# Kernel optimization log

Measured on AMD Instinct MI355X. Metric: run time of the kernel, lower is better.

## Reference

```python
import jax, jax.numpy as jnp
import numpy as np

D_HEAD = 64
KV_GROUPS = 3
KSIZE = 7


def _win_idx(L, ksize):
    # NATTEN neighborhood: window centered at i, shifted to stay in-bounds.
    start = jnp.clip(jnp.arange(L) - ksize // 2, 0, L - ksize)  # [L]
    return start[:, None] + jnp.arange(ksize)[None, :]          # [L, k]


def _natten2d(q, k, v, ksize):
    # q,k,v: [n, nh, H, W, e]; q pre-scaled.
    H, W = q.shape[2], q.shape[3]
    ih = _win_idx(H, ksize)  # [H, k]
    iw = _win_idx(W, ksize)  # [W, k]
    # gather per-query key/value windows: [n, nh, H, W, k, k, e]
    kg = k[:, :, ih[:, None, :, None], iw[None, :, None, :], :]
    vg = v[:, :, ih[:, None, :, None], iw[None, :, None, :], :]
    logits = jnp.einsum('nhije,nhijabe->nhijab', q, kg)  # [n,nh,H,W,k,k]
    n_, nh = logits.shape[:2]
    a = jax.nn.softmax(logits.reshape(n_, nh, H, W, ksize * ksize), axis=-1)
    a = a.reshape(logits.shape)
    return jnp.einsum('nhijab,nhijabe->nhije', a, vg)  # [n,nh,H,W,e]


def _to_heads(p, nh, e):
    n, h, w, _ = p.shape
    return p.reshape(n, h, w, nh, e).transpose(0, 3, 1, 2, 4)  # [n,nh,h,w,e]


def setup_inputs() -> dict:
    key = jax.random.key(0)
    k1, k2, k3 = jax.random.split(key, 3)
    x = jax.random.normal(k1, (2, 32, 32, 768), dtype=jnp.float32)
    w_qkv = jax.random.normal(k2, (1280, 768), dtype=jnp.float32) * 0.02
    w_out = jax.random.normal(k3, (768, 768), dtype=jnp.float32) * 0.02
    return {"x": x, "w_qkv": w_qkv, "w_out": w_out}


def reference(x, w_qkv, w_out):
    n, H, W, d_model = x.shape
    q_heads = d_model // D_HEAD
    kv_heads = q_heads // KV_GROUPS
    qkv = x @ w_qkv.T  # [n,H,W,1280]
    q, k, v = jnp.split(
        qkv, [q_heads * D_HEAD, (q_heads + kv_heads) * D_HEAD], axis=-1)
    q = _to_heads(q, q_heads, D_HEAD)
    k = jnp.tile(_to_heads(k, kv_heads, D_HEAD), (1, KV_GROUPS, 1, 1, 1))
    v = jnp.tile(_to_heads(v, kv_heads, D_HEAD), (1, KV_GROUPS, 1, 1, 1))
    q = q / (D_HEAD ** 0.5)
    o = _natten2d(q, k, v, KSIZE)           # [n,nh,H,W,e]
    o = o.transpose(0, 2, 3, 1, 4).reshape(n, H, W, d_model)
    return o @ w_out.T
```

## Files before the change

kernel.cpp:

```cpp
#include <hip/hip_runtime.h>
#include <hip/hip_bf16.h>


typedef __attribute__((ext_vector_type(8))) __bf16 bf16x8;
typedef __attribute__((ext_vector_type(4))) float floatx4;
typedef unsigned short u16;

__device__ inline u16 f2bf(float f) {
    union { float f; unsigned u; } v; v.f = f;
    return (u16)((v.u + 0x7fff + ((v.u >> 16) & 1)) >> 16);
}

__device__ inline void gl_lds16(const void* g, void* l) {
    __builtin_amdgcn_global_load_lds(
        (const __attribute__((address_space(1))) void*)g,
        (__attribute__((address_space(3))) void*)l, 16, 0, 0);
}

__global__ __launch_bounds__(256) void convert_kernel(
    const float* __restrict__ x, const float* __restrict__ w1,
    const float* __restrict__ w2, u16* __restrict__ xb,
    u16* __restrict__ w1b, u16* __restrict__ w2b)
{
    int t = blockIdx.x * blockDim.x + threadIdx.x;
    const float* s; u16* d;
    if (t < 393216)      { s = x;  d = xb; }
    else if (t < 638976) { s = w1; d = w1b; t -= 393216; }
    else                 { s = w2; d = w2b; t -= 638976; }
    float4 v = ((const float4*)s)[t];
    ushort4 o;
    o.x = f2bf(v.x); o.y = f2bf(v.y); o.z = f2bf(v.z); o.w = f2bf(v.w);
    ((ushort4*)d)[t] = o;
}

template<int MODE>
__global__ __launch_bounds__(256) void gemm_nt(
    const u16* __restrict__ A, const u16* __restrict__ B,
    float* __restrict__ C, u16* __restrict__ Cb, u16* __restrict__ vT,
    int M, int N, int K)
{
    __shared__ __align__(16) u16 As[4 * 64 * 32];
    __shared__ __align__(16) u16 Bs[4 * 64 * 32];
    const int tid = threadIdx.x;
    const int lane = tid & 63;
    const int wave = tid >> 6;
    const int bm = blockIdx.y * 64;
    const int bn = blockIdx.x * 64;
    const int qr = (wave >> 1) * 32;
    const int qc = (wave & 1) * 32;

    floatx4 acc[2][2] = {};

    const u16* Xsrc = (wave < 2) ? A : B;
    const int   bx  = (wave < 2) ? bm : bn;
    u16* Xlds       = (wave < 2) ? As : Bs;
    const int half  = wave & 1;
    const int l2 = lane >> 2;
    const int l3 = (lane & 3) * 8;
    const u16* gptr[8];
    u16* lptr[8];
    #pragma unroll
    for (int cc = 0; cc < 8; cc++) {
        int c = half * 8 + cc, kc = c & 3, rg = c >> 2;
        gptr[cc] = Xsrc + (size_t)(bx + rg * 16 + l2) * K + kc * 32 + l3;
        lptr[cc] = Xlds + kc * 2048 + rg * 512;
    }

    const int fr = lane & 15;
    const int fk = (lane >> 4) * 8;

    for (int k0 = 0; k0 < K; k0 += 128) {
        #pragma unroll
        for (int cc = 0; cc < 8; cc++)
            gl_lds16(gptr[cc] + k0, lptr[cc]);
        __syncthreads();
        #pragma unroll
        for (int kc = 0; kc < 4; kc++) {
            bf16x8 af0 = *(const bf16x8*)&As[kc * 2048 + (qr +      fr) * 32 + fk];
            bf16x8 af1 = *(const bf16x8*)&As[kc * 2048 + (qr + 16 + fr) * 32 + fk];
            bf16x8 bf0 = *(const bf16x8*)&Bs[kc * 2048 + (qc +      fr) * 32 + fk];
            bf16x8 bf1 = *(const bf16x8*)&Bs[kc * 2048 + (qc + 16 + fr) * 32 + fk];
            acc[0][0] = __builtin_amdgcn_mfma_f32_16x16x32_bf16(af0, bf0, acc[0][0], 0, 0, 0);
            acc[0][1] = __builtin_amdgcn_mfma_f32_16x16x32_bf16(af0, bf1, acc[0][1], 0, 0, 0);
            acc[1][0] = __builtin_amdgcn_mfma_f32_16x16x32_bf16(af1, bf0, acc[1][0], 0, 0, 0);
            acc[1][1] = __builtin_amdgcn_mfma_f32_16x16x32_bf16(af1, bf1, acc[1][1], 0, 0, 0);
        }
        __syncthreads();
    }

    const int cr = (lane >> 4) * 4;
    const int ccol = lane & 15;
    #pragma unroll
    for (int i = 0; i < 2; i++) {
        #pragma unroll
        for (int j = 0; j < 2; j++) {
            const int row0 = bm + qr + i * 16 + cr;
            const int col  = bn + qc + j * 16 + ccol;
            if (MODE == 0) {
                #pragma unroll
                for (int r = 0; r < 4; r++)
                    C[(size_t)(row0 + r) * N + col] = acc[i][j][r];
            } else {
                if (col < 1024) {
                    #pragma unroll
                    for (int r = 0; r < 4; r++)
                        Cb[(size_t)(row0 + r) * 1024 + col] = f2bf(acc[i][j][r]);
                } else {
                    ushort4 w;
                    w.x = f2bf(acc[i][j][0]); w.y = f2bf(acc[i][j][1]);
                    w.z = f2bf(acc[i][j][2]); w.w = f2bf(acc[i][j][3]);
                    *(ushort4*)&vT[(size_t)(col - 1024) * 2048 + row0] = w;
                }
            }
        }
    }
}

__global__ __launch_bounds__(256) void natten_mfma(
    const u16* __restrict__ qkv, const u16* __restrict__ vT,
    u16* __restrict__ o)
{
    __shared__ __align__(16) u16 Ks[224 * 72];
    __shared__ __align__(16) u16 Vs[64 * 224];
    __shared__ __align__(16) u16 Pw[4 * 512];
    const int h  = blockIdx.x;
    const int tb = blockIdx.y;
    const int g  = h & 3;
    const int batch = tb >> 4;
    const int ti = ((tb >> 2) & 3) * 8;
    const int tj = (tb & 3) * 8;
    const int wu_i = min(max(ti - 3, 0), 18);
    const int wu_j = min(max(tj - 3, 0), 18);
    const int tid = threadIdx.x, lane = tid & 63, wave = tid >> 6;
    const int pixbase = batch << 10;

    for (int c = tid; c < 1792; c += 256) {
        int n = c >> 3, seg = (c & 7) * 8;
        int a = n >> 4, b = min(n & 15, 13);
        int pix = pixbase + (wu_i + a) * 32 + wu_j + b;
        *(uint4*)&Ks[n * 72 + seg] =
            *(const uint4*)&qkv[(size_t)pix * 1024 + 768 + g * 64 + seg];
    }
    {
        const int b  = lane & 15;
        const int ar = lane >> 4;
        bool vok[4]; int voff[4];
        #pragma unroll
        for (int rr = 0; rr < 4; rr++) {
            int a = ar + rr * 4;
            vok[rr]  = (a < 14) && (b < 14);
            voff[rr] = (wu_i + a) * 32 + wu_j + b;
        }
        const u16* vsrc = &vT[(size_t)(g * 64 + wave * 16) * 2048 + pixbase];
        #pragma unroll 4
        for (int dd = 0; dd < 16; dd++) {
            #pragma unroll
            for (int rr = 0; rr < 4; rr++) {
                int a = ar + rr * 4;
                if (a < 14)
                    Vs[(wave * 16 + dd) * 224 + rr * 64 + lane] =
                        vok[rr] ? vsrc[voff[rr]] : (u16)0;
            }
            vsrc += 2048;
        }
    }
    __syncthreads();

    const int fr = lane & 15;
    const int fk = (lane >> 4) * 8;

    bf16x8 aq0, aq1;
    {
        int qq = wave * 16 + fr;
        int pixq = pixbase + (ti + (qq >> 3)) * 32 + tj + (qq & 7);
        const u16* qp = &qkv[(size_t)pixq * 1024 + h * 64];
        aq0 = *(const bf16x8*)(qp + fk);
        aq1 = *(const bf16x8*)(qp + 32 + fk);
    }

    bool colok[4]; int tlo[4], thi[4];
    #pragma unroll
    for (int r = 0; r < 4; r++) {
        int qq = wave * 16 + (lane >> 4) * 4 + r;
        int qi = ti + (qq >> 3), qj = tj + (qq & 7);
        int si = min(max(qi - 3, 0), 25);
        int sj = min(max(qj - 3, 0), 25);
        colok[r] = (fr < 14) && (wu_j + fr >= sj) && (wu_j + fr <= sj + 6);
        tlo[r] = si - wu_i; thi[r] = tlo[r] + 6;
    }

    float s[14][4];
    float mx[4] = {-1e30f, -1e30f, -1e30f, -1e30f};
    #pragma unroll
    for (int t = 0; t < 14; t++) {
        bf16x8 bk0 = *(const bf16x8*)&Ks[(t * 16 + fr) * 72 + fk];
        bf16x8 bk1 = *(const bf16x8*)&Ks[(t * 16 + fr) * 72 + 32 + fk];
        floatx4 a4 = {};
        a4 = __builtin_amdgcn_mfma_f32_16x16x32_bf16(aq0, bk0, a4, 0, 0, 0);
        a4 = __builtin_amdgcn_mfma_f32_16x16x32_bf16(aq1, bk1, a4, 0, 0, 0);
        #pragma unroll
        for (int r = 0; r < 4; r++) {
            bool v = colok[r] && (t >= tlo[r]) && (t <= thi[r]);
            s[t][r] = v ? a4[r] * 0.125f : -1e30f;
            mx[r] = fmaxf(mx[r], s[t][r]);
        }
    }
    #pragma unroll
    for (int r = 0; r < 4; r++) {
        mx[r] = fmaxf(mx[r], __shfl_xor(mx[r], 1));
        mx[r] = fmaxf(mx[r], __shfl_xor(mx[r], 2));
        mx[r] = fmaxf(mx[r], __shfl_xor(mx[r], 4));
        mx[r] = fmaxf(mx[r], __shfl_xor(mx[r], 8));
    }
    float l[4] = {0.f, 0.f, 0.f, 0.f};
    #pragma unroll
    for (int t = 0; t < 14; t++)
        #pragma unroll
        for (int r = 0; r < 4; r++) {
            float p = __expf(s[t][r] - mx[r]);
            s[t][r] = p; l[r] += p;
        }
    #pragma unroll
    for (int r = 0; r < 4; r++) {
        l[r] += __shfl_xor(l[r], 1);
        l[r] += __shfl_xor(l[r], 2);
        l[r] += __shfl_xor(l[r], 4);
        l[r] += __shfl_xor(l[r], 8);
    }
    float rinv[4];
    #pragma unroll
    for (int r = 0; r < 4; r++) rinv[r] = 1.0f / l[r];

    u16* pw = &Pw[wave * 512];
    floatx4 oacc[4] = {};
    #pragma unroll
    for (int kc = 0; kc < 7; kc++) {
        #pragma unroll
        for (int tt = 0; tt < 2; tt++) {
            int t = kc * 2 + tt;
            #pragma unroll
            for (int r = 0; r < 4; r++)
                pw[((lane >> 4) * 4 + r) * 32 + tt * 16 + fr] =
                    f2bf(s[t][r] * rinv[r]);
        }
        bf16x8 bp = *(const bf16x8*)&pw[fr * 32 + fk];
        #pragma unroll
        for (int u = 0; u < 4; u++) {
            bf16x8 av = *(const bf16x8*)&Vs[(u * 16 + fr) * 224 + kc * 32 + fk];
            oacc[u] = __builtin_amdgcn_mfma_f32_16x16x32_bf16(av, bp, oacc[u], 0, 0, 0);
        }
    }

    {
        int qq = wave * 16 + fr;
        int pixq = pixbase + (ti + (qq >> 3)) * 32 + tj + (qq & 7);
        u16* op = &o[(size_t)pixq * 768 + h * 64];
        #pragma unroll
        for (int u = 0; u < 4; u++) {
            ushort4 w;
            w.x = f2bf(oacc[u][0]); w.y = f2bf(oacc[u][1]);
            w.z = f2bf(oacc[u][2]); w.w = f2bf(oacc[u][3]);
            *(ushort4*)(op + u * 16 + (lane >> 4) * 4) = w;
        }
    }
}

extern "C" void kernel_launch(void* const* d_in, const int* in_sizes, int n_in,
                              void* d_out, int out_size, void* d_ws, size_t ws_size,
                              hipStream_t stream)
{
    const float* x     = (const float*)d_in[0];
    const float* w_qkv = (const float*)d_in[1];
    const float* w_out = (const float*)d_in[2];
    float* out = (float*)d_out;

    char* ws = (char*)d_ws;
    u16* qkvb = (u16*)ws; ws += (size_t)2048 * 1024 * 2;
    u16* vTb  = (u16*)ws; ws += (size_t)256 * 2048 * 2 + 64;
    u16* xb   = (u16*)ws; ws += (size_t)2048 * 768 * 2;
    u16* w1b  = (u16*)ws; ws += (size_t)1280 * 768 * 2;
    u16* w2b  = (u16*)ws; ws += (size_t)768 * 768 * 2;
    u16* ob   = (u16*)ws;

    convert_kernel<<<dim3(3072), dim3(256), 0, stream>>>(x, w_qkv, w_out, xb, w1b, w2b);

    gemm_nt<1><<<dim3(1280 / 64, 2048 / 64), dim3(256), 0, stream>>>(
        xb, w1b, nullptr, qkvb, vTb, 2048, 1280, 768);

    natten_mfma<<<dim3(12, 32), dim3(256), 0, stream>>>(qkvb, vTb, ob);

    gemm_nt<0><<<dim3(768 / 64, 2048 / 64), dim3(256), 0, stream>>>(
        ob, w2b, out, nullptr, nullptr, 2048, 768, 768);
}
```

Before: 108.7 us.

## Swap GEMM operand roles for vector stores; read NATTEN K/V from global

The QKV and output projections now pass the weight matrix as the row operand and activations as the column operand. Each lane's four accumulator values then map to consecutive output features, so the fp32 output and the bf16 Q/K section are written as float4/ushort4 vectors instead of scalar strided stores; the transposed V write becomes scalar instead. The neighborhood-attention kernel drops its LDS staging of K and V and the barrier. MFMA operands are loaded directly from global memory (K rows from qkv, V from the transposed vT buffer) over a 4-aligned 16-column window. This trades shared-memory fill and synchronisation for redundant, cache-reliant global loads across waves.

```diff
diff --git a/kernel.cpp b/kernel.cpp
--- a/kernel.cpp
+++ b/kernel.cpp
@@ -36,11 +36,11 @@
 template<int MODE>
 __global__ __launch_bounds__(256) void gemm_nt(
     const u16* __restrict__ A, const u16* __restrict__ B,
-    float* __restrict__ C, u16* __restrict__ Cb, u16* __restrict__ vT,
-    int M, int N, int K)
-{
-    __shared__ __align__(16) u16 As[4 * 64 * 32];
-    __shared__ __align__(16) u16 Bs[4 * 64 * 32];
+    float* __restrict__ out, u16* __restrict__ Cq, u16* __restrict__ vT,
+    int K)
+{
+    __shared__ __align__(16) u16 As[4 * 2048];
+    __shared__ __align__(16) u16 Bs[4 * 2048];
     const int tid = threadIdx.x;
     const int lane = tid & 63;
     const int wave = tid >> 6;
@@ -57,22 +57,22 @@
     const int half  = wave & 1;
     const int l2 = lane >> 2;
     const int l3 = (lane & 3) * 8;
-    const u16* gptr[8];
-    u16* lptr[8];
+    int gofs[8], lofs[8];
     #pragma unroll
     for (int cc = 0; cc < 8; cc++) {
         int c = half * 8 + cc, kc = c & 3, rg = c >> 2;
-        gptr[cc] = Xsrc + (size_t)(bx + rg * 16 + l2) * K + kc * 32 + l3;
-        lptr[cc] = Xlds + kc * 2048 + rg * 512;
+        gofs[cc] = (bx + rg * 16 + l2) * K + kc * 32 + l3;
+        lofs[cc] = kc * 2048 + rg * 512;
     }
 
     const int fr = lane & 15;
     const int fk = (lane >> 4) * 8;
+    const int nk = K >> 7;
 
     for (int k0 = 0; k0 < K; k0 += 128) {
         #pragma unroll
         for (int cc = 0; cc < 8; cc++)
-            gl_lds16(gptr[cc] + k0, lptr[cc]);
+            gl_lds16(Xsrc + gofs[cc] + k0, Xlds + lofs[cc]);
         __syncthreads();
         #pragma unroll
         for (int kc = 0; kc < 4; kc++) {
@@ -97,19 +97,18 @@
             const int row0 = bm + qr + i * 16 + cr;
             const int col  = bn + qc + j * 16 + ccol;
             if (MODE == 0) {
-                #pragma unroll
-                for (int r = 0; r < 4; r++)
-                    C[(size_t)(row0 + r) * N + col] = acc[i][j][r];
+                float4 w = {acc[i][j][0], acc[i][j][1], acc[i][j][2], acc[i][j][3]};
+                *(float4*)&out[(size_t)col * 768 + row0] = w;
             } else {
-                if (col < 1024) {
-                    #pragma unroll
-                    for (int r = 0; r < 4; r++)
-                        Cb[(size_t)(row0 + r) * 1024 + col] = f2bf(acc[i][j][r]);
-                } else {
+                if (row0 < 1024) {
                     ushort4 w;
                     w.x = f2bf(acc[i][j][0]); w.y = f2bf(acc[i][j][1]);
                     w.z = f2bf(acc[i][j][2]); w.w = f2bf(acc[i][j][3]);
-                    *(ushort4*)&vT[(size_t)(col - 1024) * 2048 + row0] = w;
+                    *(ushort4*)&Cq[(size_t)col * 1024 + row0] = w;
+                } else {
+                    #pragma unroll
+                    for (int r = 0; r < 4; r++)
+                        vT[(size_t)(row0 + r - 1024) * 2048 + col] = f2bf(acc[i][j][r]);
                 }
             }
         }
@@ -120,8 +119,6 @@
     const u16* __restrict__ qkv, const u16* __restrict__ vT,
     u16* __restrict__ o)
 {
-    __shared__ __align__(16) u16 Ks[224 * 72];
-    __shared__ __align__(16) u16 Vs[64 * 224];
     __shared__ __align__(16) u16 Pw[4 * 512];
     const int h  = blockIdx.x;
     const int tb = blockIdx.y;
@@ -130,41 +127,9 @@
     const int ti = ((tb >> 2) & 3) * 8;
     const int tj = (tb & 3) * 8;
     const int wu_i = min(max(ti - 3, 0), 18);
-    const int wu_j = min(max(tj - 3, 0), 18);
-    const int tid = threadIdx.x, lane = tid & 63, wave = tid >> 6;
+    const int oj   = min(max(tj - 3, 0) & ~3, 16);
+    const int lane = threadIdx.x & 63, wave = threadIdx.x >> 6;
     const int pixbase = batch << 10;
-
-    for (int c = tid; c < 1792; c += 256) {
-        int n = c >> 3, seg = (c & 7) * 8;
-        int a = n >> 4, b = min(n & 15, 13);
-        int pix = pixbase + (wu_i + a) * 32 + wu_j + b;
-        *(uint4*)&Ks[n * 72 + seg] =
-            *(const uint4*)&qkv[(size_t)pix * 1024 + 768 + g * 64 + seg];
-    }
-    {
-        const int b  = lane & 15;
-        const int ar = lane >> 4;
-        bool vok[4]; int voff[4];
-        #pragma unroll
-        for (int rr = 0; rr < 4; rr++) {
-            int a = ar + rr * 4;
-            vok[rr]  = (a < 14) && (b < 14);
-            voff[rr] = (wu_i + a) * 32 + wu_j + b;
-        }
-        const u16* vsrc = &vT[(size_t)(g * 64 + wave * 16) * 2048 + pixbase];
-        #pragma unroll 4
-        for (int dd = 0; dd < 16; dd++) {
-            #pragma unroll
-            for (int rr = 0; rr < 4; rr++) {
-                int a = ar + rr * 4;
-                if (a < 14)
-                    Vs[(wave * 16 + dd) * 224 + rr * 64 + lane] =
-                        vok[rr] ? vsrc[voff[rr]] : (u16)0;
-            }
-            vsrc += 2048;
-        }
-    }
-    __syncthreads();
 
     const int fr = lane & 15;
     const int fk = (lane >> 4) * 8;
@@ -185,7 +150,7 @@
         int qi = ti + (qq >> 3), qj = tj + (qq & 7);
         int si = min(max(qi - 3, 0), 25);
         int sj = min(max(qj - 3, 0), 25);
-        colok[r] = (fr < 14) && (wu_j + fr >= sj) && (wu_j + fr <= sj + 6);
+        colok[r] = (oj + fr >= sj) && (oj + fr <= sj + 6);
         tlo[r] = si - wu_i; thi[r] = tlo[r] + 6;
     }
 
@@ -193,8 +158,10 @@
     float mx[4] = {-1e30f, -1e30f, -1e30f, -1e30f};
     #pragma unroll
     for (int t = 0; t < 14; t++) {
-        bf16x8 bk0 = *(const bf16x8*)&Ks[(t * 16 + fr) * 72 + fk];
-        bf16x8 bk1 = *(const bf16x8*)&Ks[(t * 16 + fr) * 72 + 32 + fk];
+        int kp = pixbase + (wu_i + t) * 32 + oj + fr;
+        const u16* krow = &qkv[(size_t)kp * 1024 + 768 + g * 64];
+        bf16x8 bk0 = *(const bf16x8*)(krow + fk);
+        bf16x8 bk1 = *(const bf16x8*)(krow + 32 + fk);
         floatx4 a4 = {};
         a4 = __builtin_amdgcn_mfma_f32_16x16x32_bf16(aq0, bk0, a4, 0, 0, 0);
         a4 = __builtin_amdgcn_mfma_f32_16x16x32_bf16(aq1, bk1, a4, 0, 0, 0);
@@ -233,6 +200,8 @@
 
     u16* pw = &Pw[wave * 512];
     floatx4 oacc[4] = {};
+    const int vrow = (fk >= 16) ? 1 : 0;
+    const int vcol = oj + (fk & 8);
     #pragma unroll
     for (int kc = 0; kc < 7; kc++) {
         #pragma unroll
@@ -244,10 +213,14 @@
                     f2bf(s[t][r] * rinv[r]);
         }
         bf16x8 bp = *(const bf16x8*)&pw[fr * 32 + fk];
+        const int vpix = pixbase + (wu_i + kc * 2 + vrow) * 32 + vcol;
         #pragma unroll
         for (int u = 0; u < 4; u++) {
-            bf16x8 av = *(const bf16x8*)&Vs[(u * 16 + fr) * 224 + kc * 32 + fk];
-            oacc[u] = __builtin_amdgcn_mfma_f32_16x16x32_bf16(av, bp, oacc[u], 0, 0, 0);
+            const u16* vp = &vT[(size_t)(g * 64 + u * 16 + fr) * 2048 + vpix];
+            union { ushort4 q[2]; bf16x8 v; } av;
+            av.q[0] = *(const ushort4*)vp;
+            av.q[1] = *(const ushort4*)(vp + 4);
+            oacc[u] = __builtin_amdgcn_mfma_f32_16x16x32_bf16(av.v, bp, oacc[u], 0, 0, 0);
         }
     }
 
@@ -284,11 +257,11 @@
 
     convert_kernel<<<dim3(3072), dim3(256), 0, stream>>>(x, w_qkv, w_out, xb, w1b, w2b);
 
-    gemm_nt<1><<<dim3(1280 / 64, 2048 / 64), dim3(256), 0, stream>>>(
-        xb, w1b, nullptr, qkvb, vTb, 2048, 1280, 768);
+    gemm_nt<1><<<dim3(2048 / 64, 1280 / 64), dim3(256), 0, stream>>>(
+        w1b, xb, nullptr, qkvb, vTb, 768);
 
     natten_mfma<<<dim3(12, 32), dim3(256), 0, stream>>>(qkvb, vTb, ob);
 
-    gemm_nt<0><<<dim3(768 / 64, 2048 / 64), dim3(256), 0, stream>>>(
-        ob, w2b, out, nullptr, nullptr, 2048, 768, 768);
-}
+    gemm_nt<0><<<dim3(2048 / 64, 768 / 64), dim3(256), 0, stream>>>(
+        w2b, ob, out, nullptr, nullptr, 768);
+}
```

Measured after the change: 105.0 us. 1.04x faster.
